# Kernel tuning notes

Hardware: AMD Instinct MI355X
Metric: run time of the kernel (lower is better)

## Reference

```python
import jax, jax.numpy as jnp
import numpy as np

L, D, H, FF = 4, 256, 8, 4 * 256  # num_layers, d_model, nhead, ffn hidden
DK = D // H
EPS = 1e-5


def _ln(x, g, b):
    mu = jnp.mean(x, axis=-1, keepdims=True)
    var = jnp.mean(jnp.square(x - mu), axis=-1, keepdims=True)
    return (x - mu) * jax.lax.rsqrt(var + EPS) * g + b


def setup_inputs() -> dict:
    key = jax.random.key(0)
    ks = jax.random.split(key, 16)
    B, N = 8, 1024
    s = 0.02
    return {
        "x": jax.random.normal(ks[0], (B, N, D), jnp.float32),
        "coords": jax.random.normal(ks[1], (B, N, 3), jnp.float32),
        "Wq": jax.random.normal(ks[2], (L, D, D), jnp.float32) * s,
        "bq": jnp.zeros((L, D), jnp.float32),
        "Wk": jax.random.normal(ks[3], (L, D, D), jnp.float32) * s,
        "bk": jnp.zeros((L, D), jnp.float32),
        "Wv": jax.random.normal(ks[4], (L, D, D), jnp.float32) * s,
        "bv": jnp.zeros((L, D), jnp.float32),
        "alpha": jnp.full((L,), 0.1, jnp.float32),
        "W1": jax.random.normal(ks[5], (L, D, FF), jnp.float32) * s,
        "b1": jnp.zeros((L, FF), jnp.float32),
        "W2": jax.random.normal(ks[6], (L, FF, D), jnp.float32) * s,
        "b2": jnp.zeros((L, D), jnp.float32),
        "g1": jnp.ones((L, D), jnp.float32),
        "be1": jnp.zeros((L, D), jnp.float32),
        "g2": jnp.ones((L, D), jnp.float32),
        "be2": jnp.zeros((L, D), jnp.float32),
    }


def reference(x, coords, Wq, bq, Wk, bk, Wv, bv, alpha, W1, b1, W2, b2, g1, be1, g2, be2):
    B, N, _ = x.shape
    # Per-batch pairwise coord dot products (same math as the BN x BN matmul
    # sliced per batch in the original, computed without the cross-batch waste).
    G0 = jnp.einsum("bnc,bmc->bnm", coords, coords)  # [B,N,N]
    scale = 1.0 / jnp.sqrt(jnp.float32(DK))
    for i in range(L):
        q = (x @ Wq[i] + bq[i]).reshape(B, N, H, DK)
        k = (x @ Wk[i] + bk[i]).reshape(B, N, H, DK)
        v = (x @ Wv[i] + bv[i]).reshape(B, N, H, DK)
        scores = jnp.einsum("bnhd,bmhd->bhnm", q, k) * scale + (alpha[i] * G0)[:, None]
        attn = jax.nn.softmax(scores, axis=-1)
        out = jnp.einsum("bhnm,bmhd->bnhd", attn, v).reshape(B, N, D)
        x = _ln(x + out, g1[i], be1[i])
        ff = jnp.maximum(x @ W1[i] + b1[i], 0.0) @ W2[i] + b2[i]
        x = _ln(x + ff, g2[i], be2[i])
    return x
```

## Files before the change

### kernel.cpp

```cpp
#include <hip/hip_runtime.h>
#include <hip/hip_bf16.h>

#define BB 8
#define NN 1024
#define DD 256
#define HH 8
#define DK 32
#define FFN 1024
#define NLAYERS 4
#define MM (BB * NN)
#define ROW_ELEMS (MM * DD)

#define QSCALE 0.2550655192922103f
#define LOG2E  1.4426950408889634f

typedef unsigned short ushort_t;
typedef __attribute__((ext_vector_type(8))) short bf16x8;
typedef __attribute__((ext_vector_type(4))) short bf16x4;
typedef __attribute__((ext_vector_type(4))) float f32x4;

__device__ __forceinline__ f32x4 mfma16(bf16x4 a, bf16x4 b, f32x4 c) {
#if __has_builtin(__builtin_amdgcn_mfma_f32_16x16x16bf16_1k)
    return __builtin_amdgcn_mfma_f32_16x16x16bf16_1k(a, b, c, 0, 0, 0);
#elif defined(__AMDGCN__)
    f32x4 d;
    asm volatile("v_mfma_f32_16x16x16_bf16 %0, %1, %2, %3"
                 : "=v"(d)
                 : "v"(a), "v"(b), "v"(c));
    return d;
#else
    return c;
#endif
}

__device__ __forceinline__ ushort_t f2b(float f) {
    __hip_bfloat16 h = __float2bfloat16(f);
    return *reinterpret_cast<ushort_t*>(&h);
}

__device__ __forceinline__ float fast_exp2(float x) {
#if __has_builtin(__builtin_amdgcn_exp2f)
    return __builtin_amdgcn_exp2f(x);
#else
    return exp2f(x);
#endif
}

__device__ __forceinline__ void async_ld16(const void* g, void* l) {
    __builtin_amdgcn_global_load_lds((const __attribute__((address_space(1))) void*)g,
                                     (__attribute__((address_space(3))) void*)l, 16, 0, 0);
}

__global__ __launch_bounds__(256) void copy_in_kernel(const float4* __restrict__ in,
                                                      float4* __restrict__ xf,
                                                      ushort4* __restrict__ xb, int n4,
                                                      const float* __restrict__ coords,
                                                      ushort_t* __restrict__ Qa,
                                                      ushort_t* __restrict__ Ka) {
    int i = blockIdx.x * 256 + threadIdx.x;
    if (i < n4) {
        float4 v = in[i];
        xf[i] = v;
        ushort4 b = {f2b(v.x), f2b(v.y), f2b(v.z), f2b(v.w)};
        xb[i] = b;
    }
    if (blockIdx.x < 256) {
        const int id = blockIdx.x * 256 + threadIdx.x;
        const int bh = id >> 10, n = id & 1023;
        const int b = bh >> 3;
        ushort_t buf[32];
#pragma unroll
        for (int d = 0; d < 32; ++d) buf[d] = 0;
        buf[0] = f2b(coords[(size_t)(b * NN + n) * 3 + 0]);
        buf[1] = f2b(coords[(size_t)(b * NN + n) * 3 + 1]);
        buf[2] = f2b(coords[(size_t)(b * NN + n) * 3 + 2]);
        ushort_t* kp = Ka + ((size_t)bh * NN + n) * 64 + 32;
        ushort_t* qp = Qa + ((size_t)bh * NN + n) * 64 + 32;
        const uint4* b4 = (const uint4*)buf;
        uint4 z4 = {0u, 0u, 0u, 0u};
#pragma unroll
        for (int c = 0; c < 4; ++c) {
            *(uint4*)(kp + c * 8) = b4[c];
            *(uint4*)(qp + c * 8) = z4;
        }
    }
}

__global__ __launch_bounds__(256) void prep_kernel(const float* __restrict__ Wq,
                                                   const float* __restrict__ Wk,
                                                   const float* __restrict__ Wv,
                                                   const float* __restrict__ W1,
                                                   const float* __restrict__ W2,
                                                   const float* __restrict__ bq,
                                                   const float* __restrict__ bk,
                                                   const float* __restrict__ bv,
                                                   ushort_t* __restrict__ wqkvt,
                                                   ushort_t* __restrict__ w1t,
                                                   ushort_t* __restrict__ w2t,
                                                   float* __restrict__ bqkv) {
    const int id = blockIdx.x;
    const int layer = id / 707;
    const int r = id % 707;
    const int tid = threadIdx.x;

    if (r >= 704) {
        const int chunk = r - 704;
        const float* src = (chunk == 0) ? bq : (chunk == 1) ? bk : bv;
        bqkv[layer * 768 + chunk * 256 + tid] = src[layer * 256 + tid];
        return;
    }

    const float* src;
    ushort_t* dst;
    int R, C, x, y;
    if (r < 192) {
        const int w = r >> 6, rr = r & 63;
        src = ((w == 0) ? Wq : (w == 1) ? Wk : Wv) + (size_t)layer * 65536;
        dst = wqkvt + (size_t)layer * 196608 + w * 65536;
        R = 256; C = 256; x = rr & 7; y = rr >> 3;
    } else if (r < 448) {
        const int rr = r - 192;
        src = W1 + (size_t)layer * 262144;
        dst = w1t + (size_t)layer * 262144;
        R = 256; C = 1024; x = rr & 31; y = rr >> 5;
    } else {
        const int rr = r - 448;
        src = W2 + (size_t)layer * 262144;
        dst = w2t + (size_t)layer * 262144;
        R = 1024; C = 256; x = rr & 7; y = rr >> 3;
    }
    const int r0 = y * 32, c0 = x * 32;
    __shared__ float tile[32][33];
    const int tx = tid & 31, ty = tid >> 5;
#pragma unroll
    for (int i = 0; i < 4; ++i)
        tile[ty + 8 * i][tx] = src[(size_t)(r0 + ty + 8 * i) * C + (c0 + tx)];
    __syncthreads();
#pragma unroll
    for (int i = 0; i < 4; ++i)
        dst[(size_t)(c0 + ty + 8 * i) * R + (r0 + tx)] = f2b(tile[tx][ty + 8 * i]);
}

template <int MODE, int BM>
__global__ __launch_bounds__(256) void mfma_gemm_kernel(const ushort_t* __restrict__ A,
                                                        const ushort_t* __restrict__ Bt,
                                                        const float* __restrict__ bias,
                                                        void* __restrict__ C0,
                                                        void* __restrict__ C1,
                                                        void* __restrict__ C2,
                                                        const float* __restrict__ coords,
                                                        const float* __restrict__ alpha, int layer,
                                                        int K, int ldc) {
    constexpr int NI = BM / 32;
    __shared__ ushort_t As0[2][BM * 32];
    __shared__ ushort_t As1[2][BM * 32];
    __shared__ ushort_t Bs0[2][128 * 32];
    __shared__ ushort_t Bs1[2][128 * 32];

    const int t    = threadIdx.x;
    const int bm   = blockIdx.y * BM;
    const int bn   = blockIdx.x * 128;
    const int wave = t >> 6, lane = t & 63;
    const int wm   = (wave >> 1) * (BM / 2), wn = (wave & 1) * 64;
    const int quad = lane >> 4, l16 = lane & 15;

    const int srow = t >> 2;
    const int scol = (t & 3) * 8;

    f32x4 acc[NI][4];
#pragma unroll
    for (int i = 0; i < NI; ++i)
#pragma unroll
        for (int j = 0; j < 4; ++j) {
            f32x4 z = {0.f, 0.f, 0.f, 0.f};
            acc[i][j] = z;
        }

    auto stage = [&](int pb, int k0) {
        async_ld16(A + (size_t)(bm + srow) * K + k0 + scol, As0[pb] + wave * 512);
        if constexpr (BM == 128)
            async_ld16(A + (size_t)(bm + 64 + srow) * K + k0 + scol, As0[pb] + 2048 + wave * 512);
        async_ld16(Bt + (size_t)(bn + srow) * K + k0 + scol, Bs0[pb] + wave * 512);
        async_ld16(Bt + (size_t)(bn + 64 + srow) * K + k0 + scol, Bs0[pb] + 2048 + wave * 512);
        async_ld16(A + (size_t)(bm + srow) * K + k0 + 32 + scol, As1[pb] + wave * 512);
        if constexpr (BM == 128)
            async_ld16(A + (size_t)(bm + 64 + srow) * K + k0 + 32 + scol, As1[pb] + 2048 + wave * 512);
        async_ld16(Bt + (size_t)(bn + srow) * K + k0 + 32 + scol, Bs1[pb] + wave * 512);
        async_ld16(Bt + (size_t)(bn + 64 + srow) * K + k0 + 32 + scol, Bs1[pb] + 2048 + wave * 512);
    };

    stage(0, 0);
    int pb = 0;
    for (int k0 = 0; k0 < K; k0 += 64, pb ^= 1) {
        __syncthreads();

        if (k0 + 64 < K) stage(pb ^ 1, k0 + 64);

        bf16x8 af0[NI], af1[NI], bf0[4], bf1[4];
#pragma unroll
        for (int i = 0; i < NI; ++i) {
            af0[i] = *(const bf16x8*)(As0[pb] + (wm + i * 16 + l16) * 32 + quad * 8);
            af1[i] = *(const bf16x8*)(As1[pb] + (wm + i * 16 + l16) * 32 + quad * 8);
        }
#pragma unroll
        for (int j = 0; j < 4; ++j) {
            bf0[j] = *(const bf16x8*)(Bs0[pb] + (wn + j * 16 + l16) * 32 + quad * 8);
            bf1[j] = *(const bf16x8*)(Bs1[pb] + (wn + j * 16 + l16) * 32 + quad * 8);
        }
#pragma unroll
        for (int i = 0; i < NI; ++i)
#pragma unroll
            for (int j = 0; j < 4; ++j) {
                acc[i][j] = __builtin_amdgcn_mfma_f32_16x16x32_bf16(af0[i], bf0[j], acc[i][j], 0, 0, 0);
                acc[i][j] = __builtin_amdgcn_mfma_f32_16x16x32_bf16(af1[i], bf1[j], acc[i][j], 0, 0, 0);
            }
    }

    const float av = (MODE == 2) ? alpha[layer] : 0.f;

#pragma unroll
    for (int j = 0; j < 4; ++j) {
        const int col = bn + wn + j * 16 + l16;
        const float bsv = bias[col];
#pragma unroll
        for (int i = 0; i < NI; ++i) {
            const int row0 = bm + wm + i * 16 + quad * 4;
            if (MODE == 2) {
                const int bb2 = row0 >> 10, nn0 = row0 & 1023;
                const int which = col >> 8, rem = col & 255;
                const int h = rem >> 5, d = rem & 31;
                const size_t bh = (size_t)((bb2 << 3) + h);
                if (which == 2) {
                    ushort4 pk;
                    pk.x = f2b(acc[i][j][0] + bsv);
                    pk.y = f2b(acc[i][j][1] + bsv);
                    pk.z = f2b(acc[i][j][2] + bsv);
                    pk.w = f2b(acc[i][j][3] + bsv);
                    *(ushort4*)&((ushort_t*)C2)[(bh * DK + d) * NN + nn0] = pk;
                } else {
#pragma unroll
                    for (int r = 0; r < 4; ++r) {
                        const float v = acc[i][j][r] + bsv;
                        const int nn = nn0 + r;
                        if (which == 0) {
                            ((ushort_t*)C0)[(bh * NN + nn) * 64 + d] = f2b(v * QSCALE);
                            if (d < 3)
                                ((ushort_t*)C0)[(bh * NN + nn) * 64 + 32 + d] =
                                    f2b(av * LOG2E * coords[(size_t)(bb2 * NN + nn) * 3 + d]);
                        } else {
                            ((ushort_t*)C1)[(bh * NN + nn) * 64 + d] = f2b(v);
                        }
                    }
                }
            } else {
#pragma unroll
                for (int r = 0; r < 4; ++r) {
                    float v = acc[i][j][r] + bsv;
                    if (MODE == 0)
                        ((float*)C0)[(size_t)(row0 + r) * ldc + col] = v;
                    else
                        ((ushort_t*)C0)[(size_t)(row0 + r) * ldc + col] = f2b(fmaxf(v, 0.f));
                }
            }
        }
    }
}

__global__ __launch_bounds__(512) void ffn_ln_kernel(const float* __restrict__ aout,
                                                     const float* __restrict__ xfin,
                                                     const ushort_t* __restrict__ W1t,
                                                     const ushort_t* __restrict__ W2t,
                                                     const float* __restrict__ g1,
                                                     const float* __restrict__ be1,
                                                     const float* __restrict__ b1,
                                                     const float* __restrict__ b2,
                                                     const float* __restrict__ g2,
                                                     const float* __restrict__ be2,
                                                     float* __restrict__ xout,
                                                     ushort_t* __restrict__ xb) {
    __shared__ ushort_t Ha[8][32][32];
    __shared__ ushort_t Asf[8][32][32];
    __shared__ ushort_t Bs0[2][256 * 32];
    __shared__ ushort_t Bs1[2][256 * 32];
    __shared__ float Ya[32][260];
    __shared__ float redS[8][32];
    __shared__ float redQ[8][32];

    const int t = threadIdx.x;
    const int bm = blockIdx.x * 32;
    const int wave = t >> 6, lane = t & 63;
    const int quad = lane >> 4, l16 = lane & 15;
    const int wn = wave * 32;
    const int scol = (t & 3) * 8;

    auto stageB1 = [&](int pb, int nc, int ks) {
        const int nbase = nc * 256;
        const int k0 = ks * 64;
#pragma unroll
        for (int c = 0; c < 2; ++c) {
            const int brow = nbase + c * 128 + (t >> 2);
            async_ld16(W1t + (size_t)brow * 256 + k0 + scol, Bs0[pb] + c * 4096 + wave * 512);
            async_ld16(W1t + (size_t)brow * 256 + k0 + 32 + scol, Bs1[pb] + c * 4096 + wave * 512);
        }
    };
    auto stageB2 = [&](int pb, int nc, int ks) {
        const int k0 = nc * 256 + ks * 64;
#pragma unroll
        for (int c = 0; c < 2; ++c) {
            const int brow = c * 128 + (t >> 2);
            async_ld16(W2t + (size_t)brow * 1024 + k0 + scol, Bs0[pb] + c * 4096 + wave * 512);
            async_ld16(W2t + (size_t)brow * 1024 + k0 + 32 + scol, Bs1[pb] + c * 4096 + wave * 512);
        }
    };
    auto stage = [&](int pb, int st) {
        const int group = st >> 2, ks = st & 3, nc = group >> 1;
        if (!(group & 1)) stageB1(pb, nc, ks);
        else stageB2(pb, nc, ks);
    };

    stage(0, 0);

#pragma unroll
    for (int rr = 0; rr < 4; ++rr) {
        const int row = wave * 4 + rr;
        const size_t base = (size_t)(bm + row) * DD + lane * 4;

        float4 xv = *(const float4*)(xfin + base);
        float4 dl = *(const float4*)(aout + base);
        float v0 = xv.x + dl.x, v1 = xv.y + dl.y, v2 = xv.z + dl.z, v3 = xv.w + dl.w;

        float s = v0 + v1 + v2 + v3;
#pragma unroll
        for (int off = 32; off; off >>= 1) s += __shfl_xor(s, off);
        const float mean = s * (1.0f / 256.0f);

        float d0 = v0 - mean, d1 = v1 - mean, d2 = v2 - mean, d3 = v3 - mean;
        float s2 = d0 * d0 + d1 * d1 + d2 * d2 + d3 * d3;
#pragma unroll
        for (int off = 32; off; off >>= 1) s2 += __shfl_xor(s2, off);
        const float rs = rsqrtf(s2 * (1.0f / 256.0f) + 1e-5f);

        float4 gv = *(const float4*)(g1 + lane * 4);
        float4 bv = *(const float4*)(be1 + lane * 4);
        float y0 = d0 * rs * gv.x + bv.x;
        float y1 = d1 * rs * gv.y + bv.y;
        float y2 = d2 * rs * gv.z + bv.z;
        float y3 = d3 * rs * gv.w + bv.w;

        float4 yv = {y0, y1, y2, y3};
        *(float4*)&Ya[row][lane * 4] = yv;
        const int col0 = lane * 4;
        ushort4 yb = {f2b(y0), f2b(y1), f2b(y2), f2b(y3)};
        *(ushort4*)&Asf[col0 >> 5][row][col0 & 31] = yb;
    }

    f32x4 acc1[2][2], acc2[2][2];
#pragma unroll
    for (int i = 0; i < 2; ++i)
#pragma unroll
        for (int j = 0; j < 2; ++j) {
            f32x4 z = {0.f, 0.f, 0.f, 0.f};
            acc1[i][j] = z;
            acc2[i][j] = z;
        }

    int pb = 0;
    for (int st = 0; st < 32; ++st, pb ^= 1) {
        __syncthreads();
        if (st < 31) stage(pb ^ 1, st + 1);

        const int group = st >> 2, ks = st & 3;
        const bool ff1 = !(group & 1);

        bf16x8 af0[2], af1[2], bf0[2], bf1[2];
#pragma unroll
        for (int i = 0; i < 2; ++i) {
            if (ff1) {
                af0[i] = *(const bf16x8*)&Asf[2 * ks][i * 16 + l16][quad * 8];
                af1[i] = *(const bf16x8*)&Asf[2 * ks + 1][i * 16 + l16][quad * 8];
            } else {
                af0[i] = *(const bf16x8*)&Ha[2 * ks][i * 16 + l16][quad * 8];
                af1[i] = *(const bf16x8*)&Ha[2 * ks + 1][i * 16 + l16][quad * 8];
            }
        }
#pragma unroll
        for (int j = 0; j < 2; ++j) {
            bf0[j] = *(const bf16x8*)(Bs0[pb] + (wn + j * 16 + l16) * 32 + quad * 8);
            bf1[j] = *(const bf16x8*)(Bs1[pb] + (wn + j * 16 + l16) * 32 + quad * 8);
        }

        if (ff1) {
#pragma unroll
            for (int i = 0; i < 2; ++i)
#pragma unroll
                for (int j = 0; j < 2; ++j) {
                    acc1[i][j] = __builtin_amdgcn_mfma_f32_16x16x32_bf16(af0[i], bf0[j], acc1[i][j], 0, 0, 0);
                    acc1[i][j] = __builtin_amdgcn_mfma_f32_16x16x32_bf16(af1[i], bf1[j], acc1[i][j], 0, 0, 0);
                }
            if (ks == 3) {
                const int nc = group >> 1;
#pragma unroll
                for (int j = 0; j < 2; ++j) {
                    const int col = nc * 256 + wn + j * 16 + l16;
                    const float bj = b1[col];
#pragma unroll
                    for (int i = 0; i < 2; ++i)
#pragma unroll
                        for (int r = 0; r < 4; ++r) {
                            const int row = i * 16 + quad * 4 + r;
                            Ha[wave][row][j * 16 + l16] =
                                f2b(fmaxf(acc1[i][j][r] + bj, 0.f));
                        }
                }
#pragma unroll
                for (int i = 0; i < 2; ++i)
#pragma unroll
                    for (int j = 0; j < 2; ++j) {
                        f32x4 z = {0.f, 0.f, 0.f, 0.f};
                        acc1[i][j] = z;
                    }
            }
        } else {
#pragma unroll
            for (int i = 0; i < 2; ++i)
#pragma unroll
                for (int j = 0; j < 2; ++j) {
                    acc2[i][j] = __builtin_amdgcn_mfma_f32_16x16x32_bf16(af0[i], bf0[j], acc2[i][j], 0, 0, 0);
                    acc2[i][j] = __builtin_amdgcn_mfma_f32_16x16x32_bf16(af1[i], bf1[j], acc2[i][j], 0, 0, 0);
                }
        }
    }

    float mean[2][4], rstd[2][4];

    {
        float sum_[2][4];
#pragma unroll
        for (int i = 0; i < 2; ++i)
#pragma unroll
            for (int r = 0; r < 4; ++r) sum_[i][r] = 0.f;
#pragma unroll
        for (int j = 0; j < 2; ++j) {
            const int col = wn + j * 16 + l16;
            const float bj = b2[col];
#pragma unroll
            for (int i = 0; i < 2; ++i) {
#pragma unroll
                for (int r = 0; r < 4; ++r) {
                    const int row = i * 16 + quad * 4 + r;
                    const float v = acc2[i][j][r] + bj + Ya[row][col];
                    acc2[i][j][r] = v;
                    sum_[i][r] += v;
                }
            }
        }
#pragma unroll
        for (int i = 0; i < 2; ++i)
#pragma unroll
            for (int r = 0; r < 4; ++r) {
                float s = sum_[i][r];
                s += __shfl_xor(s, 1);
                s += __shfl_xor(s, 2);
                s += __shfl_xor(s, 4);
                s += __shfl_xor(s, 8);
                sum_[i][r] = s;
            }
        if (l16 == 0) {
#pragma unroll
            for (int i = 0; i < 2; ++i)
#pragma unroll
                for (int r = 0; r < 4; ++r) redS[wave][i * 16 + quad * 4 + r] = sum_[i][r];
        }
        __syncthreads();
#pragma unroll
        for (int i = 0; i < 2; ++i)
#pragma unroll
            for (int r = 0; r < 4; ++r) {
                const int rl = i * 16 + quad * 4 + r;
                float s = 0.f;
#pragma unroll
                for (int w = 0; w < 8; ++w) s += redS[w][rl];
                mean[i][r] = s * (1.0f / 256.0f);
            }
    }

    {
        float sq_[2][4];
#pragma unroll
        for (int i = 0; i < 2; ++i)
#pragma unroll
            for (int r = 0; r < 4; ++r) sq_[i][r] = 0.f;
#pragma unroll
        for (int j = 0; j < 2; ++j)
#pragma unroll
            for (int i = 0; i < 2; ++i)
#pragma unroll
                for (int r = 0; r < 4; ++r) {
                    const float d = acc2[i][j][r] - mean[i][r];
                    sq_[i][r] += d * d;
                }
#pragma unroll
        for (int i = 0; i < 2; ++i)
#pragma unroll
            for (int r = 0; r < 4; ++r) {
                float s = sq_[i][r];
                s += __shfl_xor(s, 1);
                s += __shfl_xor(s, 2);
                s += __shfl_xor(s, 4);
                s += __shfl_xor(s, 8);
                sq_[i][r] = s;
            }
        if (l16 == 0) {
#pragma unroll
            for (int i = 0; i < 2; ++i)
#pragma unroll
                for (int r = 0; r < 4; ++r) redQ[wave][i * 16 + quad * 4 + r] = sq_[i][r];
        }
        __syncthreads();
#pragma unroll
        for (int i = 0; i < 2; ++i)
#pragma unroll
            for (int r = 0; r < 4; ++r) {
                const int rl = i * 16 + quad * 4 + r;
                float s = 0.f;
#pragma unroll
                for (int w = 0; w < 8; ++w) s += redQ[w][rl];
                rstd[i][r] = rsqrtf(s * (1.0f / 256.0f) + 1e-5f);
            }
    }

#pragma unroll
    for (int j = 0; j < 2; ++j) {
        const int col = wn + j * 16 + l16;
        const float gv = g2[col];
        const float bev = be2[col];
#pragma unroll
        for (int i = 0; i < 2; ++i) {
            const int row = bm + i * 16 + quad * 4;
#pragma unroll
            for (int r = 0; r < 4; ++r) {
                const float y = (acc2[i][j][r] - mean[i][r]) * rstd[i][r] * gv + bev;
                xout[(size_t)(row + r) * DD + col] = y;
                xb[(size_t)(row + r) * DD + col] = f2b(y);
            }
        }
    }
}

__global__ __launch_bounds__(256, 2) void attn8_kernel(const ushort_t* __restrict__ Qa,
                                                       const ushort_t* __restrict__ Ka,
                                                       const ushort_t* __restrict__ Vt,
                                                       float* __restrict__ aout) {
    const int b = blockIdx.x, h = blockIdx.y, n0 = blockIdx.z * 64;
    const int t = threadIdx.x, wave = t >> 6, lane = t & 63;
    const int quad = lane >> 4, l16 = lane & 15;
    const int bh = b * HH + h;

    __shared__ __align__(16) char smem[56320];
    ushort_t (*Ks)[64][72] = (ushort_t (*)[64][72])smem;
    ushort_t (*Vs)[32][72] = (ushort_t (*)[32][72])(smem + 36864);
    float    (*Om)[64][36] = (float (*)[64][36])smem;
    float    (*Lm)[64]     = (float (*)[64])(smem + 55296);

    bf16x8 aq[4][2];
#pragma unroll
    for (int s = 0; s < 4; ++s) {
        const ushort_t* qp = Qa + ((size_t)bh * NN + n0 + s * 16 + l16) * 64 + quad * 8;
        aq[s][0] = *(const bf16x8*)qp;
        aq[s][1] = *(const bf16x8*)(qp + 32);
    }

    const f32x4 z = {0.f, 0.f, 0.f, 0.f};
    f32x4 acc[4][2];
    float lsum[4];
#pragma unroll
    for (int s = 0; s < 4; ++s) { acc[s][0] = z; acc[s][1] = z; lsum[s] = 0.f; }

    const ushort_t* kg = Ka + ((size_t)bh * NN + wave * 256) * 64;
    const ushort_t* vg = Vt + (size_t)bh * DK * NN + wave * 256;

    const int srow = lane >> 3, sch = (lane & 7) * 8;

    uint4 kreg[8], vreg[4];
#pragma unroll
    for (int i = 0; i < 8; ++i) kreg[i] = *(const uint4*)(kg + (size_t)(i * 8 + srow) * 64 + sch);
#pragma unroll
    for (int i = 0; i < 4; ++i) vreg[i] = *(const uint4*)(vg + (size_t)(i * 8 + srow) * NN + sch);

    for (int kt = 0; kt < 4; ++kt) {
#pragma unroll
        for (int i = 0; i < 8; ++i) *(uint4*)&Ks[wave][i * 8 + srow][sch] = kreg[i];
#pragma unroll
        for (int i = 0; i < 4; ++i) *(uint4*)&Vs[wave][i * 8 + srow][sch] = vreg[i];

        bf16x8 bk0[4], bk1[4];
#pragma unroll
        for (int jt = 0; jt < 4; ++jt) {
            bk0[jt] = *(const bf16x8*)&Ks[wave][jt * 16 + l16][quad * 8];
            bk1[jt] = *(const bf16x8*)&Ks[wave][jt * 16 + l16][32 + quad * 8];
        }
        bf16x4 vfrag[2][4];
#pragma unroll
        for (int g = 0; g < 2; ++g)
#pragma unroll
            for (int jt = 0; jt < 4; ++jt)
                vfrag[g][jt] = *(const bf16x4*)&Vs[wave][g * 16 + l16][jt * 16 + quad * 4];

        if (kt < 3) {
            const ushort_t* kg2 = kg + (size_t)(kt + 1) * 64 * 64;
            const ushort_t* vg2 = vg + (kt + 1) * 64;
#pragma unroll
            for (int i = 0; i < 8; ++i)
                kreg[i] = *(const uint4*)(kg2 + (size_t)(i * 8 + srow) * 64 + sch);
#pragma unroll
            for (int i = 0; i < 4; ++i)
                vreg[i] = *(const uint4*)(vg2 + (size_t)(i * 8 + srow) * NN + sch);
        }

#pragma unroll
        for (int s = 0; s < 4; ++s) {
            f32x4 st[4];
            __builtin_amdgcn_s_setprio(1);
#pragma unroll
            for (int jt = 0; jt < 4; ++jt) {
                st[jt] = __builtin_amdgcn_mfma_f32_16x16x32_bf16(bk0[jt], aq[s][0], z, 0, 0, 0);
                st[jt] = __builtin_amdgcn_mfma_f32_16x16x32_bf16(bk1[jt], aq[s][1], st[jt], 0, 0, 0);
            }
            __builtin_amdgcn_s_setprio(0);
            bf16x4 pf[4];
            float ls = 0.f;
#pragma unroll
            for (int jt = 0; jt < 4; ++jt) {
                float e0 = fast_exp2(st[jt][0]);
                float e1 = fast_exp2(st[jt][1]);
                float e2 = fast_exp2(st[jt][2]);
                float e3 = fast_exp2(st[jt][3]);
                ls += (e0 + e1) + (e2 + e3);
                pf[jt][0] = (short)f2b(e0);
                pf[jt][1] = (short)f2b(e1);
                pf[jt][2] = (short)f2b(e2);
                pf[jt][3] = (short)f2b(e3);
            }
            lsum[s] += ls;
            __builtin_amdgcn_s_setprio(1);
#pragma unroll
            for (int jt = 0; jt < 4; ++jt) {
                acc[s][0] = mfma16(vfrag[0][jt], pf[jt], acc[s][0]);
                acc[s][1] = mfma16(vfrag[1][jt], pf[jt], acc[s][1]);
            }
            __builtin_amdgcn_s_setprio(0);
        }
    }

#pragma unroll
    for (int s = 0; s < 4; ++s) {
        lsum[s] += __shfl_xor(lsum[s], 16);
        lsum[s] += __shfl_xor(lsum[s], 32);
    }

    __syncthreads();
    if (quad == 0) {
#pragma unroll
        for (int s = 0; s < 4; ++s) Lm[wave][s * 16 + l16] = lsum[s];
    }

#pragma unroll
    for (int s = 0; s < 4; ++s) {
        const int q = s * 16 + l16;
#pragma unroll
        for (int g = 0; g < 2; ++g) {
            float4 v = {acc[s][g][0], acc[s][g][1], acc[s][g][2], acc[s][g][3]};
            *(float4*)&Om[wave][q][g * 16 + quad * 4] = v;
        }
    }
    __syncthreads();

    {
        const int q = t >> 2, dseg = (t & 3) * 8;
        const float inv = 1.0f / (Lm[0][q] + Lm[1][q] + Lm[2][q] + Lm[3][q]);
        float* op = aout + (size_t)(b * NN + n0 + q) * DD + h * DK + dseg;
        float4 s0 = {0.f, 0.f, 0.f, 0.f}, s1 = {0.f, 0.f, 0.f, 0.f};
#pragma unroll
        for (int w = 0; w < 4; ++w) {
            float4 a = *(const float4*)&Om[w][q][dseg];
            float4 c = *(const float4*)&Om[w][q][dseg + 4];
            s0.x += a.x; s0.y += a.y; s0.z += a.z; s0.w += a.w;
            s1.x += c.x; s1.y += c.y; s1.z += c.z; s1.w += c.w;
        }
        float4 o0 = {s0.x * inv, s0.y * inv, s0.z * inv, s0.w * inv};
        float4 o1 = {s1.x * inv, s1.y * inv, s1.z * inv, s1.w * inv};
        *(float4*)op = o0;
        *(float4*)(op + 4) = o1;
    }
}

extern "C" void kernel_launch(void* const* d_in, const int* in_sizes, int n_in,
                              void* d_out, int out_size, void* d_ws, size_t ws_size,
                              hipStream_t stream) {
    const float* x      = (const float*)d_in[0];
    const float* coords = (const float*)d_in[1];
    const float* Wq     = (const float*)d_in[2];
    const float* bq     = (const float*)d_in[3];
    const float* Wk     = (const float*)d_in[4];
    const float* bk     = (const float*)d_in[5];
    const float* Wv     = (const float*)d_in[6];
    const float* bv     = (const float*)d_in[7];
    const float* alpha  = (const float*)d_in[8];
    const float* W1     = (const float*)d_in[9];
    const float* b1     = (const float*)d_in[10];
    const float* W2     = (const float*)d_in[11];
    const float* b2     = (const float*)d_in[12];
    const float* g1     = (const float*)d_in[13];
    const float* be1    = (const float*)d_in[14];
    const float* g2     = (const float*)d_in[15];
    const float* be2    = (const float*)d_in[16];

    float* ws = (float*)d_ws;
    float*    xf    = ws;
    ushort_t* xb    = (ushort_t*)(ws + 2097152);
    ushort_t* Qa    = (ushort_t*)(ws + 3145728);
    ushort_t* Ka    = (ushort_t*)(ws + 5242880);
    ushort_t* Vt    = (ushort_t*)(ws + 7340032);
    float*    aout  = ws + 8388608;
    ushort_t* wqkvt = (ushort_t*)(ws + 10485760);
    ushort_t* w1t   = (ushort_t*)(ws + 10878976);
    ushort_t* w2t   = (ushort_t*)(ws + 11403264);
    float*    bqkv  = ws + 11927552;

    prep_kernel<<<NLAYERS * 707, 256, 0, stream>>>(Wq, Wk, Wv, W1, W2, bq, bk, bv,
                                                   wqkvt, w1t, w2t, bqkv);

    copy_in_kernel<<<ROW_ELEMS / 4 / 256, 256, 0, stream>>>(
        (const float4*)x, (float4*)xf, (ushort4*)xb, ROW_ELEMS / 4, coords, Qa, Ka);

    for (int i = 0; i < NLAYERS; ++i) {
        mfma_gemm_kernel<2, 64><<<dim3(6, 128), 256, 0, stream>>>(
            xb, wqkvt + (size_t)i * 196608, bqkv + i * 768, Qa, Ka, Vt,
            coords, alpha, i, 256, 0);

        attn8_kernel<<<dim3(8, 8, 16), 256, 0, stream>>>(Qa, Ka, Vt, aout);

        ffn_ln_kernel<<<MM / 32, 512, 0, stream>>>(
            aout, xf, w1t + (size_t)i * 262144, w2t + (size_t)i * 262144,
            g1 + i * 256, be1 + i * 256, b1 + i * 1024, b2 + i * 256,
            g2 + i * 256, be2 + i * 256,
            (i == NLAYERS - 1) ? (float*)d_out : xf, xb);
    }
}
```

Measured before the change: 373.3 us.

## Fuse next layer's QKV projection into the FFN+LayerNorm kernel epilogue

The FFN/LayerNorm kernel now optionally computes the next layer's Q, K, V projection from the freshly normalized rows held in shared memory. It reuses the double-buffered weight staging and writes Qa/Ka/Vt directly. This removes the separate QKV GEMM launch for layers 1-3 and the bf16 xb round trip through global memory. In exchange, the FFN kernel gains extra MFMA work and stages, and weight reuse across rows may be lower than in the standalone GEMM tiling.

```diff
diff --git a/kernel.cpp b/kernel.cpp
--- a/kernel.cpp
+++ b/kernel.cpp
@@ -266,6 +266,7 @@
     }
 }
 
+template <int DO_QKV>
 __global__ __launch_bounds__(512) void ffn_ln_kernel(const float* __restrict__ aout,
                                                      const float* __restrict__ xfin,
                                                      const ushort_t* __restrict__ W1t,
@@ -277,7 +278,13 @@
                                                      const float* __restrict__ g2,
                                                      const float* __restrict__ be2,
                                                      float* __restrict__ xout,
-                                                     ushort_t* __restrict__ xb) {
+                                                     const ushort_t* __restrict__ Wqkvt,
+                                                     const float* __restrict__ bqkv,
+                                                     const float* __restrict__ coords,
+                                                     const float* __restrict__ alpha, int qlayer,
+                                                     ushort_t* __restrict__ Qa,
+                                                     ushort_t* __restrict__ Ka,
+                                                     ushort_t* __restrict__ Vt) {
     __shared__ ushort_t Ha[8][32][32];
     __shared__ ushort_t Asf[8][32][32];
     __shared__ ushort_t Bs0[2][256 * 32];
@@ -317,6 +324,15 @@
         if (!(group & 1)) stageB1(pb, nc, ks);
         else stageB2(pb, nc, ks);
     };
+    auto stageQKV = [&](int pb, int qst) {
+        const int chunk = qst >> 2, ks = qst & 3;
+#pragma unroll
+        for (int c = 0; c < 2; ++c) {
+            const int brow = chunk * 256 + c * 128 + (t >> 2);
+            async_ld16(Wqkvt + (size_t)brow * 256 + ks * 64 + scol, Bs0[pb] + c * 4096 + wave * 512);
+            async_ld16(Wqkvt + (size_t)brow * 256 + ks * 64 + 32 + scol, Bs1[pb] + c * 4096 + wave * 512);
+        }
+    };
 
     stage(0, 0);
 
@@ -368,6 +384,7 @@
     for (int st = 0; st < 32; ++st, pb ^= 1) {
         __syncthreads();
         if (st < 31) stage(pb ^ 1, st + 1);
+        else if (DO_QKV) stageQKV(pb ^ 1, 0);
 
         const int group = st >> 2, ks = st & 3;
         const bool ff1 = !(group & 1);
@@ -541,7 +558,91 @@
             for (int r = 0; r < 4; ++r) {
                 const float y = (acc2[i][j][r] - mean[i][r]) * rstd[i][r] * gv + bev;
                 xout[(size_t)(row + r) * DD + col] = y;
-                xb[(size_t)(row + r) * DD + col] = f2b(y);
+                if (DO_QKV)
+                    Asf[wave][i * 16 + quad * 4 + r][j * 16 + l16] = f2b(y);
+            }
+        }
+    }
+
+    if constexpr (DO_QKV) {
+        const float av = alpha[qlayer];
+        f32x4 acc3[2][2];
+#pragma unroll
+        for (int i = 0; i < 2; ++i)
+#pragma unroll
+            for (int j = 0; j < 2; ++j) {
+                f32x4 z = {0.f, 0.f, 0.f, 0.f};
+                acc3[i][j] = z;
+            }
+
+        for (int qst = 0; qst < 12; ++qst, pb ^= 1) {
+            __syncthreads();
+            if (qst < 11) stageQKV(pb ^ 1, qst + 1);
+
+            const int ks = qst & 3;
+            bf16x8 af0[2], af1[2], bf0[2], bf1[2];
+#pragma unroll
+            for (int i = 0; i < 2; ++i) {
+                af0[i] = *(const bf16x8*)&Asf[2 * ks][i * 16 + l16][quad * 8];
+                af1[i] = *(const bf16x8*)&Asf[2 * ks + 1][i * 16 + l16][quad * 8];
+            }
+#pragma unroll
+            for (int j = 0; j < 2; ++j) {
+                bf0[j] = *(const bf16x8*)(Bs0[pb] + (wn + j * 16 + l16) * 32 + quad * 8);
+                bf1[j] = *(const bf16x8*)(Bs1[pb] + (wn + j * 16 + l16) * 32 + quad * 8);
+            }
+#pragma unroll
+            for (int i = 0; i < 2; ++i)
+#pragma unroll
+                for (int j = 0; j < 2; ++j) {
+                    acc3[i][j] = __builtin_amdgcn_mfma_f32_16x16x32_bf16(af0[i], bf0[j], acc3[i][j], 0, 0, 0);
+                    acc3[i][j] = __builtin_amdgcn_mfma_f32_16x16x32_bf16(af1[i], bf1[j], acc3[i][j], 0, 0, 0);
+                }
+
+            if (ks == 3) {
+                const int which = qst >> 2;
+#pragma unroll
+                for (int j = 0; j < 2; ++j) {
+                    const int rem = wn + j * 16 + l16;
+                    const float bsv = bqkv[which * 256 + rem];
+                    const int h = rem >> 5, d = rem & 31;
+#pragma unroll
+                    for (int i = 0; i < 2; ++i) {
+                        const int row0 = bm + i * 16 + quad * 4;
+                        const int bb2 = row0 >> 10, nn0 = row0 & 1023;
+                        const size_t bh = (size_t)((bb2 << 3) + h);
+                        if (which == 2) {
+                            ushort4 pk;
+                            pk.x = f2b(acc3[i][j][0] + bsv);
+                            pk.y = f2b(acc3[i][j][1] + bsv);
+                            pk.z = f2b(acc3[i][j][2] + bsv);
+                            pk.w = f2b(acc3[i][j][3] + bsv);
+                            *(ushort4*)&Vt[(bh * DK + d) * NN + nn0] = pk;
+                        } else {
+#pragma unroll
+                            for (int r = 0; r < 4; ++r) {
+                                const float v = acc3[i][j][r] + bsv;
+                                const int nn = nn0 + r;
+                                if (which == 0) {
+                                    Qa[(bh * NN + nn) * 64 + d] = f2b(v * QSCALE);
+                                    if (d < 3)
+                                        Qa[(bh * NN + nn) * 64 + 32 + d] =
+                                            f2b(av * LOG2E *
+                                                coords[(size_t)(bb2 * NN + nn) * 3 + d]);
+                                } else {
+                                    Ka[(bh * NN + nn) * 64 + d] = f2b(v);
+                                }
+                            }
+                        }
+                    }
+                }
+#pragma unroll
+                for (int i = 0; i < 2; ++i)
+#pragma unroll
+                    for (int j = 0; j < 2; ++j) {
+                        f32x4 z = {0.f, 0.f, 0.f, 0.f};
+                        acc3[i][j] = z;
+                    }
             }
         }
     }
@@ -733,17 +834,25 @@
     copy_in_kernel<<<ROW_ELEMS / 4 / 256, 256, 0, stream>>>(
         (const float4*)x, (float4*)xf, (ushort4*)xb, ROW_ELEMS / 4, coords, Qa, Ka);
 
+    mfma_gemm_kernel<2, 64><<<dim3(6, 128), 256, 0, stream>>>(
+        xb, wqkvt, bqkv, Qa, Ka, Vt, coords, alpha, 0, 256, 0);
+
     for (int i = 0; i < NLAYERS; ++i) {
-        mfma_gemm_kernel<2, 64><<<dim3(6, 128), 256, 0, stream>>>(
-            xb, wqkvt + (size_t)i * 196608, bqkv + i * 768, Qa, Ka, Vt,
-            coords, alpha, i, 256, 0);
-
         attn8_kernel<<<dim3(8, 8, 16), 256, 0, stream>>>(Qa, Ka, Vt, aout);
 
-        ffn_ln_kernel<<<MM / 32, 512, 0, stream>>>(
-            aout, xf, w1t + (size_t)i * 262144, w2t + (size_t)i * 262144,
-            g1 + i * 256, be1 + i * 256, b1 + i * 1024, b2 + i * 256,
-            g2 + i * 256, be2 + i * 256,
-            (i == NLAYERS - 1) ? (float*)d_out : xf, xb);
-    }
-}
+        if (i < NLAYERS - 1) {
+            ffn_ln_kernel<1><<<MM / 32, 512, 0, stream>>>(
+                aout, xf, w1t + (size_t)i * 262144, w2t + (size_t)i * 262144,
+                g1 + i * 256, be1 + i * 256, b1 + i * 1024, b2 + i * 256,
+                g2 + i * 256, be2 + i * 256, xf,
+                wqkvt + (size_t)(i + 1) * 196608, bqkv + (i + 1) * 768,
+                coords, alpha, i + 1, Qa, Ka, Vt);
+        } else {
+            ffn_ln_kernel<0><<<MM / 32, 512, 0, stream>>>(
+                aout, xf, w1t + (size_t)i * 262144, w2t + (size_t)i * 262144,
+                g1 + i * 256, be1 + i * 256, b1 + i * 1024, b2 + i * 256,
+                g2 + i * 256, be2 + i * 256, (float*)d_out,
+                nullptr, nullptr, nullptr, nullptr, 0, nullptr, nullptr, nullptr);
+        }
+    }
+}
```

Measured after the change: 363.4 us. 1.03x faster.
